# Kernel tuning notes

Measured on AMD Instinct MI355X. Metric: run time of the kernel, lower is better.

## Reference

```python
import jax, jax.numpy as jnp
import numpy as np

V, T, K, L, D = 256, 256, 36, 32, 1024
TAU = 0.05
MODE = 0
NEG_INF = -jnp.inf


def setup_inputs() -> dict:
    key = jax.random.key(0)
    k1, k2 = jax.random.split(key)
    imgs = jax.random.normal(k1, (V, K, D), dtype=jnp.float32)
    caps = jax.random.normal(k2, (T, L, D), dtype=jnp.float32)
    # Full lengths: the original module writes -inf into sim and 0 into w at
    # padded positions, so padding would produce -inf*0 = NaN in the output.
    img_lens = jnp.full((V,), K, dtype=jnp.int32)
    cap_lens = jnp.full((T,), L, dtype=jnp.int32)
    return {"imgs": imgs, "caps": caps, "img_lens": img_lens, "cap_lens": cap_lens}


def _l2norm(x):
    return x / jnp.maximum(jnp.linalg.norm(x, axis=-1, keepdims=True), 1e-12)


def reference(imgs, caps, img_lens, cap_lens):
    # masks: [V,K], [T,L]
    img_mask = (jnp.arange(K)[None, :] < img_lens[:, None]).astype(imgs.dtype)
    cap_mask = (jnp.arange(L)[None, :] < cap_lens[:, None]).astype(caps.dtype)
    # AvePool: masked mean over valid tokens, then L2-normalize
    img_glo = _l2norm((imgs * img_mask[:, :, None]).sum(1) / img_lens[:, None].astype(imgs.dtype))
    cap_glo = _l2norm((caps * cap_mask[:, :, None]).sum(1) / cap_lens[:, None].astype(caps.dtype))
    # ds: [V,T,K], et: [V,T,L]  (computed as in the original; note the original
    # forward overwrites w with the masked sim, so ds/et/softmax do not affect
    # the returned value — we keep only the live dataflow here)
    ds = jnp.einsum('vkd,td->vtk', imgs, cap_glo)
    et = jnp.einsum('tld,vd->vtl', caps, img_glo)
    del ds, et  # dead in the original (w is reassigned to masked sim)
    # sim: [V,T,K,L]
    sim = jnp.einsum('vkd,tld->vtkl', imgs, caps)
    sim_mask = img_mask[:, None, :, None] * cap_mask[None, :, None, :]  # [V,T,K,L]
    valid = sim_mask != 0
    sim = jnp.where(valid, sim, NEG_INF)
    # final w in the original is sim.masked_fill(sim_mask == 0, 0)
    w = jnp.where(valid, sim, 0.0)
    return jnp.einsum('vtkl,vtkl->vt', sim, w)
```

## Files before the change

### kernel.cpp

```cpp
#include <hip/hip_runtime.h>

#define V_N 256
#define T_N 256
#define K_N 36
#define L_N 32
#define D_N 1024
#define MROWS (V_N * K_N)
#define NROWS (T_N * L_N)
#define BM 256
#define BN 256
#define BK 64
#define KSTEPS (D_N / BK)
#define NBM (MROWS / BM)
#define NBN (NROWS / BN)
#define NWG (NBM * NBN)

typedef __attribute__((ext_vector_type(8))) short bf16x8;
typedef __attribute__((ext_vector_type(4))) float f32x4;

__device__ __forceinline__ ushort f2bf(float x) {
  union { float f; unsigned int u; } c; c.f = x;
  unsigned int r = c.u + 0x7FFFu + ((c.u >> 16) & 1u);
  return (ushort)(r >> 16);
}

__global__ void cvt_cast(const float* __restrict__ imgs, const float* __restrict__ caps,
                         ushort* __restrict__ aws, ushort* __restrict__ bws) {
  const int AQ = MROWS * (D_N / 4);
  const int BQ = NROWS * (D_N / 4);
  const int total = AQ + BQ;
  for (int q = blockIdx.x * blockDim.x + threadIdx.x; q < total;
       q += gridDim.x * blockDim.x) {
    float4 f;
    ushort4* dst;
    if (q < AQ) {
      f = reinterpret_cast<const float4*>(imgs)[q];
      dst = reinterpret_cast<ushort4*>(aws) + q;
    } else {
      f = reinterpret_cast<const float4*>(caps)[q - AQ];
      dst = reinterpret_cast<ushort4*>(bws) + (q - AQ);
    }
    ushort4 u; u.x = f2bf(f.x); u.y = f2bf(f.y); u.z = f2bf(f.z); u.w = f2bf(f.w);
    *dst = u;
  }
}

__global__ __launch_bounds__(512, 2) void gemm2(
    const ushort* __restrict__ aws, const ushort* __restrict__ bws,
    float* __restrict__ out) {
  __shared__ ushort lds[2 * 2 * BM * BK];

  int orig = (int)blockIdx.x;
  int wg = (orig & 7) * (NWG / 8) + (orig >> 3);
  const int bm = wg / NBN;
  const int bn = wg % NBN;
  const int row0 = bm * BM;
  const int col0 = bn * BN;

  const int tid  = (int)threadIdx.x;
  const int lane = tid & 63;
  const int wid  = tid >> 6;
  const int wr   = wid >> 2;
  const int wc   = wid & 3;

  auto stage = [&](int kt) {
    ushort* bufA = lds + (kt & 1) * (2 * BM * BK);
    ushort* bufB = bufA + BM * BK;
#pragma unroll
    for (int it = 0; it < 4; ++it) {
      int q = it * 512 + tid;
      int r = q >> 3;
      int sw = ((q & 7) << 4) ^ ((r & 7) << 4);
      const ushort* ga = aws + (size_t)(row0 + r) * D_N + kt * BK + (sw >> 1);
      __builtin_amdgcn_global_load_lds(
          (const __attribute__((address_space(1))) void*)ga,
          (__attribute__((address_space(3))) void*)(bufA + q * 8), 16, 0, 0);
    }
#pragma unroll
    for (int it = 0; it < 4; ++it) {
      int q = it * 512 + tid;
      int r = q >> 3;
      int sw = ((q & 7) << 4) ^ ((r & 7) << 4);
      const ushort* gb = bws + (size_t)(col0 + r) * D_N + kt * BK + (sw >> 1);
      __builtin_amdgcn_global_load_lds(
          (const __attribute__((address_space(1))) void*)gb,
          (__attribute__((address_space(3))) void*)(bufB + q * 8), 16, 0, 0);
    }
  };

  f32x4 acc[8][4];
#pragma unroll
  for (int m = 0; m < 8; ++m)
#pragma unroll
    for (int n = 0; n < 4; ++n) acc[m][n] = (f32x4){0.f, 0.f, 0.f, 0.f};

  const int arow = wr * 128 + (lane & 15);
  const int brow = wc * 64 + (lane & 15);
  const int kb   = (lane >> 4) << 4;
  const int swz  = (lane & 7) << 4;

  auto compute = [&](int kt) {
    const ushort* bufA = lds + (kt & 1) * (2 * BM * BK);
    const ushort* bufB = bufA + BM * BK;
#pragma unroll
    for (int ks = 0; ks < 2; ++ks) {
      const int sw = (ks * 64 + kb) ^ swz;
      bf16x8 af[8], bf[4];
#pragma unroll
      for (int m = 0; m < 8; ++m)
        af[m] = *reinterpret_cast<const bf16x8*>(bufA + (arow + m * 16) * BK + (sw >> 1));
#pragma unroll
      for (int n = 0; n < 4; ++n)
        bf[n] = *reinterpret_cast<const bf16x8*>(bufB + (brow + n * 16) * BK + (sw >> 1));
      __builtin_amdgcn_s_setprio(1);
#pragma unroll
      for (int m = 0; m < 8; ++m)
#pragma unroll
        for (int n = 0; n < 4; ++n)
          acc[m][n] = __builtin_amdgcn_mfma_f32_16x16x32_bf16(af[m], bf[n], acc[m][n], 0, 0, 0);
      __builtin_amdgcn_s_setprio(0);
    }
  };

  stage(0);
  stage(1);
  asm volatile("s_waitcnt vmcnt(8)" ::: "memory");
  __builtin_amdgcn_sched_barrier(0);
  __builtin_amdgcn_s_barrier();
  __builtin_amdgcn_sched_barrier(0);

  for (int t = 0; t < KSTEPS - 2; ++t) {
    compute(t);
    asm volatile("s_waitcnt lgkmcnt(0)" ::: "memory");
    __builtin_amdgcn_sched_barrier(0);
    __builtin_amdgcn_s_barrier();
    __builtin_amdgcn_sched_barrier(0);
    stage(t + 2);
    asm volatile("s_waitcnt vmcnt(8)" ::: "memory");
    __builtin_amdgcn_sched_barrier(0);
    __builtin_amdgcn_s_barrier();
    __builtin_amdgcn_sched_barrier(0);
  }
  compute(KSTEPS - 2);
  asm volatile("s_waitcnt vmcnt(0)" ::: "memory");
  __builtin_amdgcn_sched_barrier(0);
  __builtin_amdgcn_s_barrier();
  __builtin_amdgcn_sched_barrier(0);
  compute(KSTEPS - 1);

#pragma unroll
  for (int m = 0; m < 8; ++m) {
    int grow = row0 + wr * 128 + m * 16;
    int v0 = grow / K_N;
    int b = (v0 + 1) * K_N;
    int rb = grow + ((lane >> 4) << 2);
#pragma unroll
    for (int np = 0; np < 2; ++np) {
      float s0 = 0.f, s1 = 0.f;
#pragma unroll
      for (int nn = 0; nn < 2; ++nn) {
        f32x4 a4 = acc[m][np * 2 + nn];
#pragma unroll
        for (int rg = 0; rg < 4; ++rg) {
          float x = a4[rg];
          float x2 = x * x;
          if (rb + rg < b) s0 += x2; else s1 += x2;
        }
      }
#pragma unroll
      for (int off = 32; off > 0; off >>= 1) {
        s0 += __shfl_xor(s0, off, 64);
        s1 += __shfl_xor(s1, off, 64);
      }
      if (lane == 0) {
        int tcol = (col0 + wc * 64 + np * 32) >> 5;
        atomicAdd(out + v0 * T_N + tcol, s0);
        if (grow + 16 > b) atomicAdd(out + (v0 + 1) * T_N + tcol, s1);
      }
    }
  }
}

__global__ __launch_bounds__(256) void gemm_fb(
    const float* __restrict__ imgs, const float* __restrict__ caps,
    float* __restrict__ out) {
  __shared__ ushort lds[128 * 64 + 128 * 64];
  ushort* ldsA = lds;
  ushort* ldsB = lds + 128 * 64;
  const int NBMf = MROWS / 128, NBNf = NROWS / 128;
  int orig = (int)blockIdx.x;
  int xcd = orig & 7;
  int idx = orig >> 3;
  int bm = xcd * (NBMf / 8) + (idx / NBNf);
  int bn = idx % NBNf;
  const int row0 = bm * 128, col0 = bn * 128;
  const int tid = (int)threadIdx.x, lane = tid & 63, wid = tid >> 6;
  const int wr = wid >> 1, wc = wid & 1;
  f32x4 acc[4][4];
#pragma unroll
  for (int i = 0; i < 4; ++i)
#pragma unroll
    for (int j = 0; j < 4; ++j) acc[i][j] = (f32x4){0.f, 0.f, 0.f, 0.f};
  for (int kt = 0; kt < KSTEPS; ++kt) {
#pragma unroll
    for (int it = 0; it < 4; ++it) {
      int q = it * 256 + tid;
      int r = q >> 3;
      int sw = ((q & 7) << 4) ^ ((r & 7) << 4);
      const float4* src = reinterpret_cast<const float4*>(
          imgs + (size_t)(row0 + r) * D_N + kt * BK + (sw >> 1));
      float4 f0 = src[0], f1 = src[1];
      union { ushort u[8]; int4 v4; } pk;
      pk.u[0] = f2bf(f0.x); pk.u[1] = f2bf(f0.y); pk.u[2] = f2bf(f0.z); pk.u[3] = f2bf(f0.w);
      pk.u[4] = f2bf(f1.x); pk.u[5] = f2bf(f1.y); pk.u[6] = f2bf(f1.z); pk.u[7] = f2bf(f1.w);
      *reinterpret_cast<int4*>(ldsA + q * 8) = pk.v4;
    }
#pragma unroll
    for (int it = 0; it < 4; ++it) {
      int q = it * 256 + tid;
      int r = q >> 3;
      int sw = ((q & 7) << 4) ^ ((r & 7) << 4);
      const float4* src = reinterpret_cast<const float4*>(
          caps + (size_t)(col0 + r) * D_N + kt * BK + (sw >> 1));
      float4 f0 = src[0], f1 = src[1];
      union { ushort u[8]; int4 v4; } pk;
      pk.u[0] = f2bf(f0.x); pk.u[1] = f2bf(f0.y); pk.u[2] = f2bf(f0.z); pk.u[3] = f2bf(f0.w);
      pk.u[4] = f2bf(f1.x); pk.u[5] = f2bf(f1.y); pk.u[6] = f2bf(f1.z); pk.u[7] = f2bf(f1.w);
      *reinterpret_cast<int4*>(ldsB + q * 8) = pk.v4;
    }
    __syncthreads();
#pragma unroll
    for (int ks = 0; ks < 2; ++ks) {
      bf16x8 afr[4], bfr[4];
#pragma unroll
      for (int i = 0; i < 4; ++i) {
        int r = wr * 64 + i * 16 + (lane & 15);
        int sw = (ks * 64 + (((lane >> 4) << 4))) ^ ((r & 7) << 4);
        afr[i] = *reinterpret_cast<const bf16x8*>(ldsA + r * BK + (sw >> 1));
      }
#pragma unroll
      for (int j = 0; j < 4; ++j) {
        int r = wc * 64 + j * 16 + (lane & 15);
        int sw = (ks * 64 + (((lane >> 4) << 4))) ^ ((r & 7) << 4);
        bfr[j] = *reinterpret_cast<const bf16x8*>(ldsB + r * BK + (sw >> 1));
      }
#pragma unroll
      for (int i = 0; i < 4; ++i)
#pragma unroll
        for (int j = 0; j < 4; ++j)
          acc[i][j] = __builtin_amdgcn_mfma_f32_16x16x32_bf16(afr[i], bfr[j], acc[i][j], 0, 0, 0);
    }
    __syncthreads();
  }
#pragma unroll
  for (int i = 0; i < 4; ++i) {
#pragma unroll
    for (int j = 0; j < 4; ++j) {
      f32x4 a4 = acc[i][j];
      int grow = row0 + wr * 64 + i * 16;
      int gcol = col0 + wc * 64 + j * 16;
      int t = gcol >> 5;
      int v0 = grow / K_N;
      int b = (v0 + 1) * K_N;
      int rbase = grow + ((lane >> 4) << 2);
      float s0 = 0.f, s1 = 0.f;
#pragma unroll
      for (int rg = 0; rg < 4; ++rg) {
        float x = a4[rg];
        float x2 = x * x;
        if (rbase + rg < b) s0 += x2; else s1 += x2;
      }
#pragma unroll
      for (int off = 32; off > 0; off >>= 1) {
        s0 += __shfl_xor(s0, off, 64);
        s1 += __shfl_xor(s1, off, 64);
      }
      if (lane == 0) {
        atomicAdd(out + v0 * T_N + t, s0);
        if (b < grow + 16) atomicAdd(out + (v0 + 1) * T_N + t, s1);
      }
    }
  }
}

extern "C" void kernel_launch(void* const* d_in, const int* in_sizes, int n_in,
                              void* d_out, int out_size, void* d_ws, size_t ws_size,
                              hipStream_t stream) {
  const float* imgs = (const float*)d_in[0];
  const float* caps = (const float*)d_in[1];
  float* out = (float*)d_out;

  hipMemsetAsync(d_out, 0, (size_t)V_N * T_N * sizeof(float), stream);

  const size_t need = (size_t)(MROWS + NROWS) * D_N * sizeof(ushort);

  if (ws_size >= need) {
    ushort* aws = (ushort*)d_ws;
    ushort* bws = aws + (size_t)MROWS * D_N;
    cvt_cast<<<2048, 256, 0, stream>>>(imgs, caps, aws, bws);
    gemm2<<<NWG, 512, 0, stream>>>(aws, bws, out);
  } else {
    const int nwg = (MROWS / 128) * (NROWS / 128);
    gemm_fb<<<nwg, 256, 0, stream>>>(imgs, caps, out);
  }
}
```

Measured before the change: 200.4 us.

## Overlap next-tile global loads with last MFMA quarter inside each k-tile

Restructures the main loop so each k-tile first loads all A/B fragments for both k-substeps into registers. It then runs three quarters of the MFMAs, waits on LDS and barriers, issues the global-to-LDS staging for tile t+2, and finishes the last MFMA quarter. The aim is to hide the barrier and load-issue latency behind matrix work, where before staging ran between compute phases. It raises register pressure by holding a0/a1/b0/b1 at once, which may cause spills at launch bounds 512x2.

New measurement: 197.8 us. No clear change (-1.3%).

```diff
diff --git a/kernel.cpp b/kernel.cpp
--- a/kernel.cpp
+++ b/kernel.cpp
@@ -63,9 +63,8 @@
   const int wr   = wid >> 2;
   const int wc   = wid & 3;
 
-  auto stage = [&](int kt) {
+  auto stageA = [&](int kt) {
     ushort* bufA = lds + (kt & 1) * (2 * BM * BK);
-    ushort* bufB = bufA + BM * BK;
 #pragma unroll
     for (int it = 0; it < 4; ++it) {
       int q = it * 512 + tid;
@@ -76,6 +75,9 @@
           (const __attribute__((address_space(1))) void*)ga,
           (__attribute__((address_space(3))) void*)(bufA + q * 8), 16, 0, 0);
     }
+  };
+  auto stageB = [&](int kt) {
+    ushort* bufB = lds + (kt & 1) * (2 * BM * BK) + BM * BK;
 #pragma unroll
     for (int it = 0; it < 4; ++it) {
       int q = it * 512 + tid;
@@ -99,54 +101,90 @@
   const int kb   = (lane >> 4) << 4;
   const int swz  = (lane & 7) << 4;
 
-  auto compute = [&](int kt) {
-    const ushort* bufA = lds + (kt & 1) * (2 * BM * BK);
+  auto tile = [&](int t, int do_stage) {
+    const ushort* bufA = lds + (t & 1) * (2 * BM * BK);
     const ushort* bufB = bufA + BM * BK;
-#pragma unroll
-    for (int ks = 0; ks < 2; ++ks) {
-      const int sw = (ks * 64 + kb) ^ swz;
-      bf16x8 af[8], bf[4];
-#pragma unroll
-      for (int m = 0; m < 8; ++m)
-        af[m] = *reinterpret_cast<const bf16x8*>(bufA + (arow + m * 16) * BK + (sw >> 1));
+    const int sw0 = (kb) ^ swz;
+    const int sw1 = (64 + kb) ^ swz;
+
+    bf16x8 a0[8], a1[8], b0[4], b1[4];
+#pragma unroll
+    for (int m = 0; m < 4; ++m)
+      a0[m] = *reinterpret_cast<const bf16x8*>(bufA + (arow + m * 16) * BK + (sw0 >> 1));
+#pragma unroll
+    for (int n = 0; n < 4; ++n)
+      b0[n] = *reinterpret_cast<const bf16x8*>(bufB + (brow + n * 16) * BK + (sw0 >> 1));
+#pragma unroll
+    for (int m = 4; m < 8; ++m)
+      a0[m] = *reinterpret_cast<const bf16x8*>(bufA + (arow + m * 16) * BK + (sw0 >> 1));
+#pragma unroll
+    for (int m = 0; m < 4; ++m)
+      a1[m] = *reinterpret_cast<const bf16x8*>(bufA + (arow + m * 16) * BK + (sw1 >> 1));
+#pragma unroll
+    for (int n = 0; n < 4; ++n)
+      b1[n] = *reinterpret_cast<const bf16x8*>(bufB + (brow + n * 16) * BK + (sw1 >> 1));
+#pragma unroll
+    for (int m = 4; m < 8; ++m)
+      a1[m] = *reinterpret_cast<const bf16x8*>(bufA + (arow + m * 16) * BK + (sw1 >> 1));
+
+    __builtin_amdgcn_s_setprio(1);
+#pragma unroll
+    for (int m = 0; m < 4; ++m)
 #pragma unroll
       for (int n = 0; n < 4; ++n)
-        bf[n] = *reinterpret_cast<const bf16x8*>(bufB + (brow + n * 16) * BK + (sw >> 1));
-      __builtin_amdgcn_s_setprio(1);
-#pragma unroll
-      for (int m = 0; m < 8; ++m)
-#pragma unroll
-        for (int n = 0; n < 4; ++n)
-          acc[m][n] = __builtin_amdgcn_mfma_f32_16x16x32_bf16(af[m], bf[n], acc[m][n], 0, 0, 0);
-      __builtin_amdgcn_s_setprio(0);
-    }
+        acc[m][n] = __builtin_amdgcn_mfma_f32_16x16x32_bf16(a0[m], b0[n], acc[m][n], 0, 0, 0);
+    __builtin_amdgcn_s_setprio(0);
+    __builtin_amdgcn_s_setprio(1);
+#pragma unroll
+    for (int m = 4; m < 8; ++m)
+#pragma unroll
+      for (int n = 0; n < 4; ++n)
+        acc[m][n] = __builtin_amdgcn_mfma_f32_16x16x32_bf16(a0[m], b0[n], acc[m][n], 0, 0, 0);
+    __builtin_amdgcn_s_setprio(0);
+    __builtin_amdgcn_s_setprio(1);
+#pragma unroll
+    for (int m = 0; m < 4; ++m)
+#pragma unroll
+      for (int n = 0; n < 4; ++n)
+        acc[m][n] = __builtin_amdgcn_mfma_f32_16x16x32_bf16(a1[m], b1[n], acc[m][n], 0, 0, 0);
+    __builtin_amdgcn_s_setprio(0);
+
+    asm volatile("s_waitcnt lgkmcnt(0)" ::: "memory");
+    __builtin_amdgcn_sched_barrier(0);
+    __builtin_amdgcn_s_barrier();
+    __builtin_amdgcn_sched_barrier(0);
+
+    if (do_stage) { stageA(t + 2); stageB(t + 2); }
+
+    __builtin_amdgcn_s_setprio(1);
+#pragma unroll
+    for (int m = 4; m < 8; ++m)
+#pragma unroll
+      for (int n = 0; n < 4; ++n)
+        acc[m][n] = __builtin_amdgcn_mfma_f32_16x16x32_bf16(a1[m], b1[n], acc[m][n], 0, 0, 0);
+    __builtin_amdgcn_s_setprio(0);
   };
 
-  stage(0);
-  stage(1);
+  stageA(0); stageB(0);
+  stageA(1); stageB(1);
   asm volatile("s_waitcnt vmcnt(8)" ::: "memory");
   __builtin_amdgcn_sched_barrier(0);
   __builtin_amdgcn_s_barrier();
   __builtin_amdgcn_sched_barrier(0);
 
   for (int t = 0; t < KSTEPS - 2; ++t) {
-    compute(t);
-    asm volatile("s_waitcnt lgkmcnt(0)" ::: "memory");
-    __builtin_amdgcn_sched_barrier(0);
-    __builtin_amdgcn_s_barrier();
-    __builtin_amdgcn_sched_barrier(0);
-    stage(t + 2);
+    tile(t, 1);
     asm volatile("s_waitcnt vmcnt(8)" ::: "memory");
     __builtin_amdgcn_sched_barrier(0);
     __builtin_amdgcn_s_barrier();
     __builtin_amdgcn_sched_barrier(0);
   }
-  compute(KSTEPS - 2);
+  tile(KSTEPS - 2, 0);
   asm volatile("s_waitcnt vmcnt(0)" ::: "memory");
   __builtin_amdgcn_sched_barrier(0);
   __builtin_amdgcn_s_barrier();
   __builtin_amdgcn_sched_barrier(0);
-  compute(KSTEPS - 1);
+  tile(KSTEPS - 1, 0);
 
 #pragma unroll
   for (int m = 0; m < 8; ++m) {
```

## Load B fragments directly from global to registers and remap blocks per XCD

Applied to the files above, without the earlier changes.

The main GEMM kernel stops staging the B (caption) tile through LDS. Each wave reads its B fragments straight from global memory into registers every K-step, which halves LDS usage and removes the B LDS writes and reads. Only A stays double-buffered in LDS, and the wait counts are adjusted to match. The block-to-tile mapping in both kernels is changed so each XCD owns a contiguous slice of B columns, aiming for better L2 reuse of B. The trade-off is that the B global loads are not prefetched, so their latency sits on the critical path each iteration, and B rows are fetched redundantly by the two wave rows.

Measured after the change: 280.2 us. 39.9% more time.

```diff
diff --git a/kernel.cpp b/kernel.cpp
--- a/kernel.cpp
+++ b/kernel.cpp
@@ -17,6 +17,9 @@
 
 typedef __attribute__((ext_vector_type(8))) short bf16x8;
 typedef __attribute__((ext_vector_type(4))) float f32x4;
+
+#define SB0 __builtin_amdgcn_sched_barrier(0)
+#define BAR __builtin_amdgcn_s_barrier()
 
 __device__ __forceinline__ ushort f2bf(float x) {
   union { float f; unsigned int u; } c; c.f = x;
@@ -48,12 +51,13 @@
 __global__ __launch_bounds__(512, 2) void gemm2(
     const ushort* __restrict__ aws, const ushort* __restrict__ bws,
     float* __restrict__ out) {
-  __shared__ ushort lds[2 * 2 * BM * BK];
+  __shared__ ushort lds[2 * BM * BK];
 
   int orig = (int)blockIdx.x;
-  int wg = (orig & 7) * (NWG / 8) + (orig >> 3);
-  const int bm = wg / NBN;
-  const int bn = wg % NBN;
+  int xcd = orig & 7;
+  int idx = orig >> 3;
+  const int bn = xcd * 4 + (idx & 3);
+  const int bm = idx >> 2;
   const int row0 = bm * BM;
   const int col0 = bn * BN;
 
@@ -63,9 +67,10 @@
   const int wr   = wid >> 2;
   const int wc   = wid & 3;
 
-  auto stage = [&](int kt) {
-    ushort* bufA = lds + (kt & 1) * (2 * BM * BK);
-    ushort* bufB = bufA + BM * BK;
+  const int kb  = (lane >> 4) << 4;
+
+  auto stageA = [&](int kt) {
+    ushort* bufA = lds + (kt & 1) * (BM * BK);
 #pragma unroll
     for (int it = 0; it < 4; ++it) {
       int q = it * 512 + tid;
@@ -76,77 +81,63 @@
           (const __attribute__((address_space(1))) void*)ga,
           (__attribute__((address_space(3))) void*)(bufA + q * 8), 16, 0, 0);
     }
-#pragma unroll
-    for (int it = 0; it < 4; ++it) {
-      int q = it * 512 + tid;
-      int r = q >> 3;
-      int sw = ((q & 7) << 4) ^ ((r & 7) << 4);
-      const ushort* gb = bws + (size_t)(col0 + r) * D_N + kt * BK + (sw >> 1);
-      __builtin_amdgcn_global_load_lds(
-          (const __attribute__((address_space(1))) void*)gb,
-          (__attribute__((address_space(3))) void*)(bufB + q * 8), 16, 0, 0);
-    }
   };
 
+  auto rdA = [&](const ushort* bufA, int m, int ks) -> bf16x8 {
+    int r = wr * 128 + m * 16 + (lane & 15);
+    int sw = (ks * 64 + kb) ^ ((r & 7) << 4);
+    return *reinterpret_cast<const bf16x8*>(bufA + r * BK + (sw >> 1));
+  };
+
+  const ushort* bbase = bws + (size_t)(col0 + wc * 64 + (lane & 15)) * D_N
+                        + ((lane >> 4) << 3);
+
   f32x4 acc[8][4];
 #pragma unroll
   for (int m = 0; m < 8; ++m)
 #pragma unroll
     for (int n = 0; n < 4; ++n) acc[m][n] = (f32x4){0.f, 0.f, 0.f, 0.f};
 
-  const int arow = wr * 128 + (lane & 15);
-  const int brow = wc * 64 + (lane & 15);
-  const int kb   = (lane >> 4) << 4;
-  const int swz  = (lane & 7) << 4;
-
-  auto compute = [&](int kt) {
-    const ushort* bufA = lds + (kt & 1) * (2 * BM * BK);
-    const ushort* bufB = bufA + BM * BK;
-#pragma unroll
-    for (int ks = 0; ks < 2; ++ks) {
-      const int sw = (ks * 64 + kb) ^ swz;
-      bf16x8 af[8], bf[4];
-#pragma unroll
-      for (int m = 0; m < 8; ++m)
-        af[m] = *reinterpret_cast<const bf16x8*>(bufA + (arow + m * 16) * BK + (sw >> 1));
-#pragma unroll
-      for (int n = 0; n < 4; ++n)
-        bf[n] = *reinterpret_cast<const bf16x8*>(bufB + (brow + n * 16) * BK + (sw >> 1));
-      __builtin_amdgcn_s_setprio(1);
-#pragma unroll
-      for (int m = 0; m < 8; ++m)
-#pragma unroll
-        for (int n = 0; n < 4; ++n)
-          acc[m][n] = __builtin_amdgcn_mfma_f32_16x16x32_bf16(af[m], bf[n], acc[m][n], 0, 0, 0);
-      __builtin_amdgcn_s_setprio(0);
-    }
-  };
-
-  stage(0);
-  stage(1);
-  asm volatile("s_waitcnt vmcnt(8)" ::: "memory");
-  __builtin_amdgcn_sched_barrier(0);
-  __builtin_amdgcn_s_barrier();
-  __builtin_amdgcn_sched_barrier(0);
-
-  for (int t = 0; t < KSTEPS - 2; ++t) {
-    compute(t);
-    asm volatile("s_waitcnt lgkmcnt(0)" ::: "memory");
-    __builtin_amdgcn_sched_barrier(0);
-    __builtin_amdgcn_s_barrier();
-    __builtin_amdgcn_sched_barrier(0);
-    stage(t + 2);
-    asm volatile("s_waitcnt vmcnt(8)" ::: "memory");
-    __builtin_amdgcn_sched_barrier(0);
-    __builtin_amdgcn_s_barrier();
-    __builtin_amdgcn_sched_barrier(0);
-  }
-  compute(KSTEPS - 2);
-  asm volatile("s_waitcnt vmcnt(0)" ::: "memory");
-  __builtin_amdgcn_sched_barrier(0);
-  __builtin_amdgcn_s_barrier();
-  __builtin_amdgcn_sched_barrier(0);
-  compute(KSTEPS - 1);
+  stageA(0);
+  stageA(1);
+  asm volatile("s_waitcnt vmcnt(4)" ::: "memory");
+  SB0; BAR; SB0;
+
+  for (int t = 0; t < KSTEPS; ++t) {
+    const ushort* bufA = lds + (t & 1) * (BM * BK);
+
+    bf16x8 bfr[8];
+#pragma unroll
+    for (int n = 0; n < 4; ++n) {
+      const ushort* bp = bbase + (size_t)n * 16 * D_N + t * BK;
+      bfr[n]     = *reinterpret_cast<const bf16x8*>(bp);
+      bfr[4 + n] = *reinterpret_cast<const bf16x8*>(bp + 32);
+    }
+
+    bf16x8 aA0[8], aA1[8];
+#pragma unroll
+    for (int m = 0; m < 8; ++m) { aA0[m] = rdA(bufA, m, 0); aA1[m] = rdA(bufA, m, 1); }
+
+    __builtin_amdgcn_s_setprio(1);
+#pragma unroll
+    for (int m = 0; m < 8; ++m)
+#pragma unroll
+      for (int n = 0; n < 4; ++n) {
+        acc[m][n] = __builtin_amdgcn_mfma_f32_16x16x32_bf16(aA0[m], bfr[n], acc[m][n], 0, 0, 0);
+        acc[m][n] = __builtin_amdgcn_mfma_f32_16x16x32_bf16(aA1[m], bfr[4 + n], acc[m][n], 0, 0, 0);
+      }
+    __builtin_amdgcn_s_setprio(0);
+
+    if (t <= KSTEPS - 3) {
+      SB0; BAR; SB0;
+      stageA(t + 2);
+      asm volatile("s_waitcnt vmcnt(4)" ::: "memory");
+      SB0; BAR; SB0;
+    } else if (t == KSTEPS - 2) {
+      asm volatile("s_waitcnt vmcnt(0)" ::: "memory");
+      SB0; BAR; SB0;
+    }
+  }
 
 #pragma unroll
   for (int m = 0; m < 8; ++m) {
@@ -191,8 +182,8 @@
   int orig = (int)blockIdx.x;
   int xcd = orig & 7;
   int idx = orig >> 3;
-  int bm = xcd * (NBMf / 8) + (idx / NBNf);
-  int bn = idx % NBNf;
+  int bn = xcd * (NBNf / 8) + (idx % (NBNf / 8));
+  int bm = idx / (NBNf / 8);
   const int row0 = bm * 128, col0 = bn * 128;
   const int tid = (int)threadIdx.x, lane = tid & 63, wid = tid >> 6;
   const int wr = wid >> 1, wc = wid & 1;
```
